# Kernel optimization log

Hardware: AMD Instinct MI355X
Metric: run time of the kernel (lower is better)

Reference implementation:

```python
import jax, jax.numpy as jnp
import numpy as np

EMBED_DIM = 1024
N_HEADS = 16
HEAD_DIM = EMBED_DIM // N_HEADS


def setup_inputs() -> dict:
    key = jax.random.key(0)
    k1, k2, k3 = jax.random.split(key, 3)
    B, T, D = 2, 2048, EMBED_DIM
    x = jax.random.normal(k1, (B, T, D), dtype=jnp.float32)
    # torch nn.Linear weights: (out_features, in_features); y = x @ W.T
    scale = 1.0 / np.sqrt(D)
    qkv_w = jax.random.uniform(k2, (3 * D, D), dtype=jnp.float32, minval=-scale, maxval=scale)
    out_w = jax.random.uniform(k3, (D, D), dtype=jnp.float32, minval=-scale, maxval=scale)
    return {"x": x, "qkv_w": qkv_w, "out_w": out_w}


def reference(x, qkv_w, out_w):
    B, T, D = x.shape
    H, hd = N_HEADS, HEAD_DIM
    qkv = jnp.einsum('btd,ed->bte', x, qkv_w)  # (B,T,3D)
    qkv = qkv.reshape(B, T, 3, H, hd)
    q = jnp.transpose(qkv[:, :, 0], (0, 2, 1, 3))  # (B,H,T,hd)
    k = jnp.transpose(qkv[:, :, 1], (0, 2, 1, 3))
    v = jnp.transpose(qkv[:, :, 2], (0, 2, 1, 3))
    scores = jnp.einsum('bhtd,bhsd->bhts', q, k) / np.sqrt(hd).astype(np.float32)
    causal = jnp.tril(jnp.ones((T, T), dtype=bool))  # True = keep
    scores = jnp.where(causal[None, None], scores, -jnp.inf)
    probs = jax.nn.softmax(scores, axis=-1)
    out = jnp.einsum('bhts,bhsd->bhtd', probs, v)
    out = jnp.transpose(out, (0, 2, 1, 3)).reshape(B, T, D)
    return jnp.einsum('btd,ed->bte', out, out_w)
```

## Files before the change

kernel.cpp:

```cpp
#include <hip/hip_runtime.h>
#include <stdint.h>

typedef __bf16 bf16;
typedef __attribute__((ext_vector_type(8))) __bf16 bf16x8;
typedef __attribute__((ext_vector_type(4))) __bf16 bf16x4;
typedef __attribute__((ext_vector_type(4))) float f32x4;

#define AS1 __attribute__((address_space(1)))
#define AS3 __attribute__((address_space(3)))

__device__ __forceinline__ void async16(const void* g, void* l) {
  __builtin_amdgcn_global_load_lds((AS1 uint32_t*)(g), (AS3 uint32_t*)(l), 16, 0, 0);
}

__device__ __forceinline__ f32x4 mfma_bf16(bf16x8 a, bf16x8 b, f32x4 c) {
  return __builtin_amdgcn_mfma_f32_16x16x32_bf16(a, b, c, 0, 0, 0);
}

__device__ __forceinline__ uint32_t pack_bf16(float a, float b) {
  union { bf16 h[2]; uint32_t u; } u;
  u.h[0] = (bf16)a; u.h[1] = (bf16)b;
  return u.u;
}

__global__ __launch_bounds__(256) void cast_all_kernel(
    const float* __restrict__ x, const float* __restrict__ w1,
    const float* __restrict__ w2, bf16* __restrict__ xb,
    bf16* __restrict__ w1b, bf16* __restrict__ w2b) {
  const int bid = blockIdx.x;
  const float* src;
  bf16* dst;
  int base;
  if (bid < 4096) { src = x;  dst = xb;  base = bid; }
  else if (bid < 7168) { src = w1; dst = w1b; base = bid - 4096; }
  else { src = w2; dst = w2b; base = bid - 7168; }
  const int i = (base * 256 + threadIdx.x) * 4;
  const float4 v = *(const float4*)(src + i);
  bf16x4 o;
  o[0] = (bf16)v.x; o[1] = (bf16)v.y; o[2] = (bf16)v.z; o[3] = (bf16)v.w;
  *(bf16x4*)(dst + i) = o;
}

__global__ __launch_bounds__(256) void gemm_qkv_kernel(
    const bf16* __restrict__ A, const bf16* __restrict__ W,
    bf16* __restrict__ QK, bf16* __restrict__ VT) {
  constexpr int K = 1024;
  __shared__ __align__(16) bf16 sm[2 * 128 * 32];
  const int tid = threadIdx.x;
  const int w = tid >> 6, lane = tid & 63;
  const int m0 = blockIdx.x * 128, n0 = blockIdx.y * 128;
  const int wm = (w >> 1) * 64, wn = (w & 1) * 64;
  const int lrow = lane & 15, quad = lane >> 4;
  const int lk = quad * 8;
  f32x4 acc[4][4] = {};

  for (int k0 = 0; k0 < K; k0 += 32) {
#pragma unroll
    for (int i = 0; i < 4; ++i) {
      const int c = tid + 256 * i;
      const bf16* src = (c < 512)
          ? (A + (size_t)(m0 + (c >> 2)) * K + k0 + (c & 3) * 8)
          : (W + (size_t)(n0 + ((c - 512) >> 2)) * K + k0 + (c & 3) * 8);
      async16(src, sm + (w * 64 + i * 256) * 8);
    }
    __syncthreads();
    bf16x8 af[4], bfr[4];
#pragma unroll
    for (int mi = 0; mi < 4; ++mi)
      af[mi] = *(const bf16x8*)&sm[(wm + mi * 16 + lrow) * 32 + lk];
#pragma unroll
    for (int ni = 0; ni < 4; ++ni)
      bfr[ni] = *(const bf16x8*)&sm[128 * 32 + (wn + ni * 16 + lrow) * 32 + lk];
#pragma unroll
    for (int mi = 0; mi < 4; ++mi)
#pragma unroll
      for (int ni = 0; ni < 4; ++ni)
        acc[mi][ni] = mfma_bf16(af[mi], bfr[ni], acc[mi][ni]);
    __syncthreads();
  }

  bf16* s2 = sm;
  const bool isV = (n0 >= 2048);
  const int bb = m0 >> 11;
  const int mt = m0 & 2047;
  if (!isV) {
#pragma unroll
    for (int c = 0; c < 2; ++c) {
      if ((w >> 1) == c) {
#pragma unroll
        for (int mi = 0; mi < 4; ++mi)
#pragma unroll
          for (int ni = 0; ni < 4; ++ni) {
            const int nr = wn + ni * 16 + lrow;
#pragma unroll
            for (int r = 0; r < 4; ++r)
              s2[(mi * 16 + quad * 4 + r) * 128 + nr] = (bf16)acc[mi][ni][r];
          }
      }
      __syncthreads();
#pragma unroll
      for (int p = 0; p < 4; ++p) {
        const int row = p * 16 + (tid >> 4);
        const int colc = (tid & 15) * 8;
        const bf16x8 v = *(const bf16x8*)&s2[row * 128 + colc];
        *(bf16x8*)(QK + (size_t)(m0 + c * 64 + row) * 2048 + n0 + colc) = v;
      }
      __syncthreads();
    }
  } else {
#pragma unroll
    for (int c = 0; c < 2; ++c) {
      if ((w & 1) == c) {
#pragma unroll
        for (int mi = 0; mi < 4; ++mi)
#pragma unroll
          for (int ni = 0; ni < 4; ++ni) {
            const int nl = ni * 16 + lrow;
            bf16x4 pk4;
#pragma unroll
            for (int r = 0; r < 4; ++r) pk4[r] = (bf16)acc[mi][ni][r];
            *(bf16x4*)&s2[nl * 128 + wm + mi * 16 + quad * 4] = pk4;
          }
      }
      __syncthreads();
#pragma unroll
      for (int p = 0; p < 4; ++p) {
        const int row = p * 16 + (tid >> 4);
        const int colc = (tid & 15) * 8;
        const bf16x8 v = *(const bf16x8*)&s2[row * 128 + colc];
        const int vtrow = bb * 1024 + (n0 - 2048) + c * 64 + row;
        *(bf16x8*)(VT + (size_t)vtrow * 2048 + mt + colc) = v;
      }
      __syncthreads();
    }
  }
}

__global__ __launch_bounds__(256) void attn_kernel(
    const bf16* __restrict__ QK, const bf16* __restrict__ VT,
    bf16* __restrict__ AO) {
  __shared__ __align__(16) bf16 sK[2][64 * 64];
  __shared__ __align__(16) bf16 sV[2][64 * 64];
  const int bh = blockIdx.x;
  const int qt = 31 - blockIdx.y;
  const int b = bh >> 4, h = bh & 15;
  const int tid = threadIdx.x, w = tid >> 6, lane = tid & 63;
  const int q0 = qt * 64;
  const int col = lane & 15, quad = lane >> 4;
  const bf16* Qb = QK + (size_t)b * 2048 * 2048 + h * 64;
  const bf16* Kb = Qb + 1024;
  const bf16* Vb = VT + (size_t)bh * 64 * 2048;
  const float NEG_INF = -__builtin_inff();
  constexpr float QSCALE = 0.18033688011112042f;
  constexpr float FMX = 16.0f;

  const int qrow = q0 + w * 16 + col;
  bf16x8 qf[2];
#pragma unroll
  for (int kk = 0; kk < 2; ++kk) {
    bf16x8 v = *(const bf16x8*)(Qb + (size_t)qrow * 2048 + kk * 32 + quad * 8);
#pragma unroll
    for (int e = 0; e < 8; ++e) v[e] = (bf16)((float)v[e] * QSCALE);
    qf[kk] = v;
  }

  auto stage = [&](int buf, int s0) {
#pragma unroll
    for (int i = 0; i < 2; ++i) {
      const int L = tid + 256 * i;
      const int row = L >> 3;
      const int ch = (L & 7) ^ (row & 7);
      async16(Kb + (size_t)(s0 + row) * 2048 + ch * 8, &sK[buf][L * 8]);
    }
#pragma unroll
    for (int i = 0; i < 2; ++i) {
      const int L = tid + 256 * i;
      const int row = L >> 3;
      const int ch = (L & 7) ^ (row & 7);
      async16(Vb + (size_t)row * 2048 + s0 + ch * 8, &sV[buf][L * 8]);
    }
  };

  f32x4 accO[4] = {};
  float l_part = 0.f;
  const int lane0 = ((quad & 1) * 2) * 16 + col;
  const int lane1 = lane0 + 16;
  const bool hiM = (quad >> 1) != 0;

  stage(0, 0);

  auto body = [&](int kt, bool masked) {
    const int s0 = kt * 64;
    const bf16* kbuf = sK[kt & 1];
    const bf16* vbuf = sV[kt & 1];

    f32x4 st[4] = {};
#pragma unroll
    for (int kk = 0; kk < 2; ++kk) {
      bf16x8 kf[4];
#pragma unroll
      for (int m = 0; m < 4; ++m) {
        const int row = m * 16 + col;
        kf[m] = *(const bf16x8*)&kbuf[row * 64 + (((kk * 4 + quad) ^ (row & 7)) * 8)];
      }
#pragma unroll
      for (int m = 0; m < 4; ++m)
        st[m] = mfma_bf16(kf[m], qf[kk], st[m]);
    }

    if (masked) {
      const int qg = qrow;
#pragma unroll
      for (int m = 0; m < 4; ++m)
#pragma unroll
        for (int r = 0; r < 4; ++r) {
          const int kv = s0 + m * 16 + quad * 4 + r;
          st[m][r] = (kv <= qg) ? st[m][r] : NEG_INF;
        }
    }

    float rs = 0.f;
    uint32_t pk[4][2];
#pragma unroll
    for (int m = 0; m < 4; ++m) {
      const float p0 = __builtin_amdgcn_exp2f(st[m][0] - FMX);
      const float p1 = __builtin_amdgcn_exp2f(st[m][1] - FMX);
      const float p2 = __builtin_amdgcn_exp2f(st[m][2] - FMX);
      const float p3 = __builtin_amdgcn_exp2f(st[m][3] - FMX);
      rs += (p0 + p1) + (p2 + p3);
      pk[m][0] = pack_bf16(p0, p1);
      pk[m][1] = pack_bf16(p2, p3);
    }
    l_part += rs;

#pragma unroll
    for (int kk = 0; kk < 2; ++kk) {
      const uint32_t a0 = (uint32_t)__shfl((int)pk[2 * kk][0], lane0);
      const uint32_t b0 = (uint32_t)__shfl((int)pk[2 * kk + 1][0], lane0);
      const uint32_t a1 = (uint32_t)__shfl((int)pk[2 * kk][1], lane0);
      const uint32_t b1 = (uint32_t)__shfl((int)pk[2 * kk + 1][1], lane0);
      const uint32_t a2 = (uint32_t)__shfl((int)pk[2 * kk][0], lane1);
      const uint32_t b2 = (uint32_t)__shfl((int)pk[2 * kk + 1][0], lane1);
      const uint32_t a3 = (uint32_t)__shfl((int)pk[2 * kk][1], lane1);
      const uint32_t b3 = (uint32_t)__shfl((int)pk[2 * kk + 1][1], lane1);
      union { uint32_t u[4]; bf16x8 v; } f;
      f.u[0] = hiM ? b0 : a0;
      f.u[1] = hiM ? b1 : a1;
      f.u[2] = hiM ? b2 : a2;
      f.u[3] = hiM ? b3 : a3;
      bf16x8 vf[4];
#pragma unroll
      for (int d = 0; d < 4; ++d) {
        const int row = d * 16 + col;
        vf[d] = *(const bf16x8*)&vbuf[row * 64 + (((kk * 4 + quad) ^ (row & 7)) * 8)];
      }
#pragma unroll
      for (int d = 0; d < 4; ++d)
        accO[d] = mfma_bf16(vf[d], f.v, accO[d]);
    }
  };

  for (int kt = 0; kt < qt; ++kt) {
    __syncthreads();
    stage((kt + 1) & 1, (kt + 1) * 64);
    body(kt, false);
  }
  __syncthreads();
  body(qt, true);

  float rs = l_part;
  rs += __shfl_xor(rs, 16);
  rs += __shfl_xor(rs, 32);
  const float inv = 1.0f / rs;
  bf16* Ob = AO + (size_t)b * 2048 * 1024 + h * 64;
#pragma unroll
  for (int d = 0; d < 4; ++d) {
    bf16x4 o;
#pragma unroll
    for (int r = 0; r < 4; ++r) o[r] = (bf16)(accO[d][r] * inv);
    *(bf16x4*)(Ob + (size_t)qrow * 1024 + d * 16 + quad * 4) = o;
  }
}

__global__ __launch_bounds__(256) void gemm_out_kernel(
    const bf16* __restrict__ A, const bf16* __restrict__ W,
    float* __restrict__ C) {
  constexpr int K = 1024;
  __shared__ __align__(16) bf16 sm[2 * 128 * 32];
  const int tid = threadIdx.x;
  const int w = tid >> 6, lane = tid & 63;
  const int m0 = blockIdx.x * 128, n0 = blockIdx.y * 128;
  const int wm = (w >> 1) * 64, wn = (w & 1) * 64;
  const int lrow = lane & 15, lk = (lane >> 4) * 8;
  f32x4 acc[4][4] = {};

  for (int k0 = 0; k0 < K; k0 += 32) {
#pragma unroll
    for (int i = 0; i < 4; ++i) {
      const int c = tid + 256 * i;
      const bf16* src = (c < 512)
          ? (A + (size_t)(m0 + (c >> 2)) * K + k0 + (c & 3) * 8)
          : (W + (size_t)(n0 + ((c - 512) >> 2)) * K + k0 + (c & 3) * 8);
      async16(src, sm + (w * 64 + i * 256) * 8);
    }
    __syncthreads();
    bf16x8 af[4], bfr[4];
#pragma unroll
    for (int mi = 0; mi < 4; ++mi)
      af[mi] = *(const bf16x8*)&sm[(wm + mi * 16 + lrow) * 32 + lk];
#pragma unroll
    for (int ni = 0; ni < 4; ++ni)
      bfr[ni] = *(const bf16x8*)&sm[128 * 32 + (wn + ni * 16 + lrow) * 32 + lk];
#pragma unroll
    for (int mi = 0; mi < 4; ++mi)
#pragma unroll
      for (int ni = 0; ni < 4; ++ni)
        acc[mi][ni] = mfma_bf16(af[mi], bfr[ni], acc[mi][ni]);
    __syncthreads();
  }

#pragma unroll
  for (int mi = 0; mi < 4; ++mi)
#pragma unroll
    for (int ni = 0; ni < 4; ++ni) {
      const int n = n0 + wn + ni * 16 + lrow;
#pragma unroll
      for (int r = 0; r < 4; ++r) {
        const int m = m0 + wm + mi * 16 + (lane >> 4) * 4 + r;
        C[(size_t)m * 1024 + n] = acc[mi][ni][r];
      }
    }
}

extern "C" void kernel_launch(void* const* d_in, const int* in_sizes, int n_in,
                              void* d_out, int out_size, void* d_ws, size_t ws_size,
                              hipStream_t stream) {
  const float* x     = (const float*)d_in[0];
  const float* qkv_w = (const float*)d_in[1];
  const float* out_w = (const float*)d_in[2];
  float* out = (float*)d_out;

  char* ws = (char*)d_ws;
  bf16* xb    = (bf16*)(ws);
  bf16* aob   = (bf16*)(ws);
  bf16* wqkvb = (bf16*)(ws + 8u * 1024 * 1024);
  bf16* wob   = (bf16*)(ws + 14u * 1024 * 1024);
  bf16* qkb   = (bf16*)(ws + 16u * 1024 * 1024);
  bf16* vtb   = (bf16*)(ws + 32u * 1024 * 1024);

  cast_all_kernel<<<8192, 256, 0, stream>>>(x, qkv_w, out_w, xb, wqkvb, wob);
  gemm_qkv_kernel<<<dim3(32, 24), 256, 0, stream>>>(xb, wqkvb, qkb, vtb);
  attn_kernel<<<dim3(32, 32), 256, 0, stream>>>(qkb, vtb, aob);
  gemm_out_kernel<<<dim3(32, 8), 256, 0, stream>>>(aob, wob, out);
}
```

Baseline: 177.6 us.

## Give each attention wave two query tiles and remap K rows to drop shuffles

The attention kernel now runs 128 threads per block, so each of 2 waves handles 32 query rows as two 16-row tiles. Every K and V fragment read from LDS is reused for two MFMAs. K rows are loaded in a permuted order (srow), so the S-tile output layout already matches the B-operand layout for the PV MFMA, which removes the eight cross-lane shuffles per k-step. The trade-off is higher register pressure from the doubled accumulators and fewer waves per block to hide latency.

New measurement: 183.7 us. 3.4% more time.

```diff
diff --git a/kernel.cpp b/kernel.cpp
--- a/kernel.cpp
+++ b/kernel.cpp
@@ -136,7 +136,7 @@
   }
 }
 
-__global__ __launch_bounds__(256) void attn_kernel(
+__global__ __launch_bounds__(128) void attn_kernel(
     const bf16* __restrict__ QK, const bf16* __restrict__ VT,
     bf16* __restrict__ AO) {
   __shared__ __align__(16) bf16 sK[2][64 * 64];
@@ -154,38 +154,44 @@
   constexpr float QSCALE = 0.18033688011112042f;
   constexpr float FMX = 16.0f;
 
-  const int qrow = q0 + w * 16 + col;
-  bf16x8 qf[2];
-#pragma unroll
-  for (int kk = 0; kk < 2; ++kk) {
-    bf16x8 v = *(const bf16x8*)(Qb + (size_t)qrow * 2048 + kk * 32 + quad * 8);
-#pragma unroll
-    for (int e = 0; e < 8; ++e) v[e] = (bf16)((float)v[e] * QSCALE);
-    qf[kk] = v;
+  int qrow[2];
+  bf16x8 qf[2][2];
+#pragma unroll
+  for (int qtile = 0; qtile < 2; ++qtile) {
+    qrow[qtile] = q0 + w * 32 + qtile * 16 + col;
+#pragma unroll
+    for (int kk = 0; kk < 2; ++kk) {
+      bf16x8 v = *(const bf16x8*)(Qb + (size_t)qrow[qtile] * 2048 + kk * 32 + quad * 8);
+#pragma unroll
+      for (int e = 0; e < 8; ++e) v[e] = (bf16)((float)v[e] * QSCALE);
+      qf[qtile][kk] = v;
+    }
   }
 
   auto stage = [&](int buf, int s0) {
 #pragma unroll
-    for (int i = 0; i < 2; ++i) {
-      const int L = tid + 256 * i;
+    for (int i = 0; i < 4; ++i) {
+      const int L = tid + 128 * i;
       const int row = L >> 3;
       const int ch = (L & 7) ^ (row & 7);
       async16(Kb + (size_t)(s0 + row) * 2048 + ch * 8, &sK[buf][L * 8]);
     }
 #pragma unroll
-    for (int i = 0; i < 2; ++i) {
-      const int L = tid + 256 * i;
+    for (int i = 0; i < 4; ++i) {
+      const int L = tid + 128 * i;
       const int row = L >> 3;
       const int ch = (L & 7) ^ (row & 7);
       async16(Vb + (size_t)row * 2048 + s0 + ch * 8, &sV[buf][L * 8]);
     }
   };
 
-  f32x4 accO[4] = {};
-  float l_part = 0.f;
-  const int lane0 = ((quad & 1) * 2) * 16 + col;
-  const int lane1 = lane0 + 16;
-  const bool hiM = (quad >> 1) != 0;
+  int srow[4];
+#pragma unroll
+  for (int m = 0; m < 4; ++m)
+    srow[m] = 32 * (m & 1) + (col >> 2) * 8 + 4 * (m >> 1) + (col & 3);
+
+  f32x4 accO[4][2] = {};
+  float l_part[2] = {0.f, 0.f};
 
   stage(0, 0);
 
@@ -194,60 +200,51 @@
     const bf16* kbuf = sK[kt & 1];
     const bf16* vbuf = sV[kt & 1];
 
-    f32x4 st[4] = {};
+    f32x4 st[2][4] = {};
 #pragma unroll
     for (int kk = 0; kk < 2; ++kk) {
       bf16x8 kf[4];
 #pragma unroll
+      for (int m = 0; m < 4; ++m)
+        kf[m] = *(const bf16x8*)&kbuf[srow[m] * 64 + (((kk * 4 + quad) ^ (srow[m] & 7)) * 8)];
+#pragma unroll
+      for (int m = 0; m < 4; ++m)
+#pragma unroll
+        for (int qtile = 0; qtile < 2; ++qtile)
+          st[qtile][m] = mfma_bf16(kf[m], qf[qtile][kk], st[qtile][m]);
+    }
+
+    if (masked) {
+#pragma unroll
+      for (int qtile = 0; qtile < 2; ++qtile)
+#pragma unroll
+        for (int m = 0; m < 4; ++m) {
+          const int kvb = s0 + 32 * (m & 1) + quad * 8 + 4 * (m >> 1);
+#pragma unroll
+          for (int r = 0; r < 4; ++r)
+            st[qtile][m][r] = (kvb + r <= qrow[qtile]) ? st[qtile][m][r] : NEG_INF;
+        }
+    }
+
+    uint32_t pk[2][4][2];
+#pragma unroll
+    for (int qtile = 0; qtile < 2; ++qtile) {
+      float rs = 0.f;
+#pragma unroll
       for (int m = 0; m < 4; ++m) {
-        const int row = m * 16 + col;
-        kf[m] = *(const bf16x8*)&kbuf[row * 64 + (((kk * 4 + quad) ^ (row & 7)) * 8)];
-      }
-#pragma unroll
-      for (int m = 0; m < 4; ++m)
-        st[m] = mfma_bf16(kf[m], qf[kk], st[m]);
-    }
-
-    if (masked) {
-      const int qg = qrow;
-#pragma unroll
-      for (int m = 0; m < 4; ++m)
-#pragma unroll
-        for (int r = 0; r < 4; ++r) {
-          const int kv = s0 + m * 16 + quad * 4 + r;
-          st[m][r] = (kv <= qg) ? st[m][r] : NEG_INF;
-        }
-    }
-
-    float rs = 0.f;
-    uint32_t pk[4][2];
-#pragma unroll
-    for (int m = 0; m < 4; ++m) {
-      const float p0 = __builtin_amdgcn_exp2f(st[m][0] - FMX);
-      const float p1 = __builtin_amdgcn_exp2f(st[m][1] - FMX);
-      const float p2 = __builtin_amdgcn_exp2f(st[m][2] - FMX);
-      const float p3 = __builtin_amdgcn_exp2f(st[m][3] - FMX);
-      rs += (p0 + p1) + (p2 + p3);
-      pk[m][0] = pack_bf16(p0, p1);
-      pk[m][1] = pack_bf16(p2, p3);
-    }
-    l_part += rs;
+        const float p0 = __builtin_amdgcn_exp2f(st[qtile][m][0] - FMX);
+        const float p1 = __builtin_amdgcn_exp2f(st[qtile][m][1] - FMX);
+        const float p2 = __builtin_amdgcn_exp2f(st[qtile][m][2] - FMX);
+        const float p3 = __builtin_amdgcn_exp2f(st[qtile][m][3] - FMX);
+        rs += (p0 + p1) + (p2 + p3);
+        pk[qtile][m][0] = pack_bf16(p0, p1);
+        pk[qtile][m][1] = pack_bf16(p2, p3);
+      }
+      l_part[qtile] += rs;
+    }
 
 #pragma unroll
     for (int kk = 0; kk < 2; ++kk) {
-      const uint32_t a0 = (uint32_t)__shfl((int)pk[2 * kk][0], lane0);
-      const uint32_t b0 = (uint32_t)__shfl((int)pk[2 * kk + 1][0], lane0);
-      const uint32_t a1 = (uint32_t)__shfl((int)pk[2 * kk][1], lane0);
-      const uint32_t b1 = (uint32_t)__shfl((int)pk[2 * kk + 1][1], lane0);
-      const uint32_t a2 = (uint32_t)__shfl((int)pk[2 * kk][0], lane1);
-      const uint32_t b2 = (uint32_t)__shfl((int)pk[2 * kk + 1][0], lane1);
-      const uint32_t a3 = (uint32_t)__shfl((int)pk[2 * kk][1], lane1);
-      const uint32_t b3 = (uint32_t)__shfl((int)pk[2 * kk + 1][1], lane1);
-      union { uint32_t u[4]; bf16x8 v; } f;
-      f.u[0] = hiM ? b0 : a0;
-      f.u[1] = hiM ? b1 : a1;
-      f.u[2] = hiM ? b2 : a2;
-      f.u[3] = hiM ? b3 : a3;
       bf16x8 vf[4];
 #pragma unroll
       for (int d = 0; d < 4; ++d) {
@@ -255,8 +252,16 @@
         vf[d] = *(const bf16x8*)&vbuf[row * 64 + (((kk * 4 + quad) ^ (row & 7)) * 8)];
       }
 #pragma unroll
-      for (int d = 0; d < 4; ++d)
-        accO[d] = mfma_bf16(vf[d], f.v, accO[d]);
+      for (int qtile = 0; qtile < 2; ++qtile) {
+        union { uint32_t u[4]; bf16x8 v; } f;
+        f.u[0] = pk[qtile][kk][0];
+        f.u[1] = pk[qtile][kk][1];
+        f.u[2] = pk[qtile][2 + kk][0];
+        f.u[3] = pk[qtile][2 + kk][1];
+#pragma unroll
+        for (int d = 0; d < 4; ++d)
+          accO[d][qtile] = mfma_bf16(vf[d], f.v, accO[d][qtile]);
+      }
     }
   };
 
@@ -268,17 +273,20 @@
   __syncthreads();
   body(qt, true);
 
-  float rs = l_part;
-  rs += __shfl_xor(rs, 16);
-  rs += __shfl_xor(rs, 32);
-  const float inv = 1.0f / rs;
   bf16* Ob = AO + (size_t)b * 2048 * 1024 + h * 64;
 #pragma unroll
-  for (int d = 0; d < 4; ++d) {
-    bf16x4 o;
-#pragma unroll
-    for (int r = 0; r < 4; ++r) o[r] = (bf16)(accO[d][r] * inv);
-    *(bf16x4*)(Ob + (size_t)qrow * 1024 + d * 16 + quad * 4) = o;
+  for (int qtile = 0; qtile < 2; ++qtile) {
+    float rs = l_part[qtile];
+    rs += __shfl_xor(rs, 16);
+    rs += __shfl_xor(rs, 32);
+    const float inv = 1.0f / rs;
+#pragma unroll
+    for (int d = 0; d < 4; ++d) {
+      bf16x4 o;
+#pragma unroll
+      for (int r = 0; r < 4; ++r) o[r] = (bf16)(accO[d][qtile][r] * inv);
+      *(bf16x4*)(Ob + (size_t)qrow[qtile] * 1024 + d * 16 + quad * 4) = o;
+    }
   }
 }
 
@@ -350,6 +358,6 @@
 
   cast_all_kernel<<<8192, 256, 0, stream>>>(x, qkv_w, out_w, xb, wqkvb, wob);
   gemm_qkv_kernel<<<dim3(32, 24), 256, 0, stream>>>(xb, wqkvb, qkb, vtb);
-  attn_kernel<<<dim3(32, 32), 256, 0, stream>>>(qkb, vtb, aob);
+  attn_kernel<<<dim3(32, 32), 128, 0, stream>>>(qkb, vtb, aob);
   gemm_out_kernel<<<dim3(32, 8), 256, 0, stream>>>(aob, wob, out);
 }
```
